# Kernel tuning notes

Hardware: AMD Instinct MI355X
Metric: run time of the kernel (lower is better)

Reference implementation:

```python
import jax, jax.numpy as jnp
import numpy as np

BATCH, NSTEPS, IN_F, OUT_F = 8192, 16, 256, 512


def setup_inputs() -> dict:
    key = jax.random.key(0)
    ks = jax.random.split(key, 20)
    r = jax.random.normal
    return {
        "x": r(ks[0], (BATCH, NSTEPS, IN_F), jnp.float32),
        "C": r(ks[1], (BATCH, OUT_F, 1), jnp.float32),
        "H": r(ks[2], (BATCH, OUT_F, 1), jnp.float32),
        "fg_w_c": r(ks[3], (OUT_F, 1), jnp.float32),
        "fg_w_h": r(ks[4], (OUT_F, OUT_F), jnp.float32),
        "fg_w_x": r(ks[5], (OUT_F, IN_F), jnp.float32),
        "fg_b": r(ks[6], (OUT_F, 1), jnp.float32),
        "ig_w_c": r(ks[7], (OUT_F, 1), jnp.float32),
        "ig_w_h": r(ks[8], (OUT_F, OUT_F), jnp.float32),
        "ig_w_x": r(ks[9], (OUT_F, IN_F), jnp.float32),
        "ig_b": r(ks[10], (OUT_F, 1), jnp.float32),
        "in_w_h": r(ks[11], (OUT_F, OUT_F), jnp.float32),
        "in_w_x": r(ks[12], (OUT_F, IN_F), jnp.float32),
        "in_b": r(ks[13], (OUT_F, 1), jnp.float32),
        "og_w_cn": r(ks[14], (OUT_F, 1), jnp.float32),
        "og_w_h": r(ks[15], (OUT_F, OUT_F), jnp.float32),
        "og_w_x": r(ks[16], (OUT_F, IN_F), jnp.float32),
        "og_b": r(ks[17], (OUT_F, 1), jnp.float32),
        "n": 3,
    }


def reference(x, C, H,
              fg_w_c, fg_w_h, fg_w_x, fg_b,
              ig_w_c, ig_w_h, ig_w_x, ig_b,
              in_w_h, in_w_x, in_b,
              og_w_cn, og_w_h, og_w_x, og_b,
              n):
    # x: [B, T, IN] -> current step [B, IN, 1]
    x_cur = x[:, n, :, None]
    # peephole LSTM gates; matmul broadcasts [O,O] @ [B,O,1] -> [B,O,1]
    fg = jax.nn.sigmoid(fg_w_c * C + jnp.matmul(fg_w_h, H) + jnp.matmul(fg_w_x, x_cur) + fg_b)
    ig = jax.nn.sigmoid(ig_w_c * C + jnp.matmul(ig_w_h, H) + jnp.matmul(ig_w_x, x_cur) + ig_b)
    inn = jnp.tanh(jnp.matmul(in_w_h, H) + jnp.matmul(in_w_x, x_cur) + in_b)
    cm = fg * C + ig * inn
    og = jax.nn.sigmoid(og_w_cn * cm + jnp.matmul(og_w_h, H) + jnp.matmul(og_w_x, x_cur) + og_b)
    h = og * jnp.tanh(cm)
    return (cm, h)
```

## Files before the change

kernel.cpp:

```cpp
#include <hip/hip_runtime.h>


typedef _Float16 half8 __attribute__((ext_vector_type(8)));
typedef _Float16 half4v __attribute__((ext_vector_type(4)));
typedef float floatx4 __attribute__((ext_vector_type(4)));

#define BATCH 8192
#define NSTEPS 16
#define IN_F 256
#define OUT_F 512
#define KDIM 768
#define NDIM 2048

#define BM 128
#define BN 128
#define BK 64

__device__ __forceinline__ void async_copy16(const void* gptr, void* lptr) {
  __builtin_amdgcn_global_load_lds(
      (const __attribute__((address_space(1))) unsigned int*)gptr,
      (__attribute__((address_space(3))) unsigned int*)lptr,
      16, 0, 0);
}

__device__ __forceinline__ float sigmoidf_(float x) {
  return 1.0f / (1.0f + __expf(-x));
}

__device__ __forceinline__ float tanhf_(float x) {
  x = fminf(fmaxf(x, -20.0f), 20.0f);
  float e = __expf(2.0f * x);
  return (e - 1.0f) / (e + 1.0f);
}

__global__ void pack_A(const float* __restrict__ H, const float* __restrict__ x,
                       const int* __restrict__ nptr, _Float16* __restrict__ A) {
  const int n = *nptr;
  const int b = blockIdx.x;
  const int k = threadIdx.x * 4;
  float4 v;
  if (k < OUT_F)
    v = *(const float4*)(H + (size_t)b * OUT_F + k);
  else
    v = *(const float4*)(x + ((size_t)b * NSTEPS + n) * IN_F + (k - OUT_F));
  half4v h = {(_Float16)v.x, (_Float16)v.y, (_Float16)v.z, (_Float16)v.w};
  *(half4v*)(A + (size_t)b * KDIM + k) = h;
}

__global__ void pack_W(const float* __restrict__ fg_w_h, const float* __restrict__ fg_w_x,
                       const float* __restrict__ ig_w_h, const float* __restrict__ ig_w_x,
                       const float* __restrict__ in_w_h, const float* __restrict__ in_w_x,
                       const float* __restrict__ og_w_h, const float* __restrict__ og_w_x,
                       _Float16* __restrict__ W) {
  const int row = blockIdx.x;
  const int g = row >> 9;
  const int j = row & 511;
  const int k = threadIdx.x * 4;
  const float* src;
  if (k < OUT_F) {
    const float* wh = (g == 0) ? fg_w_h : (g == 1) ? ig_w_h : (g == 2) ? in_w_h : og_w_h;
    src = wh + (size_t)j * OUT_F + k;
  } else {
    const float* wx = (g == 0) ? fg_w_x : (g == 1) ? ig_w_x : (g == 2) ? in_w_x : og_w_x;
    src = wx + (size_t)j * IN_F + (k - OUT_F);
  }
  float4 v = *(const float4*)src;
  half4v h = {(_Float16)v.x, (_Float16)v.y, (_Float16)v.z, (_Float16)v.w};
  *(half4v*)(W + (size_t)row * KDIM + k) = h;
}

__global__ __launch_bounds__(256) void gemm_f16(const _Float16* __restrict__ A,
                                                const _Float16* __restrict__ W,
                                                float* __restrict__ Z) {
  __shared__ __align__(16) _Float16 As[BM * BK];
  __shared__ __align__(16) _Float16 Bs[BN * BK];

  const int tid = threadIdx.x;
  const int lane = tid & 63;
  const int wave = tid >> 6;
  const int quad = lane >> 4;
  const int l16 = lane & 15;
  const int m0 = blockIdx.y * BM;
  const int n0 = blockIdx.x * BN;
  const int mw = (wave >> 1) * 64;
  const int nw = (wave & 1) * 64;

  floatx4 acc[4][4] = {};

  for (int kt = 0; kt < KDIM; kt += BK) {
    __syncthreads();
#pragma unroll
    for (int r = 0; r < 4; ++r) {
      const int g = r * 256 + tid;
      const int row = g >> 3;
      const int cl = g & 7;
      const int cg = cl ^ (row & 7);
      async_copy16(A + (size_t)(m0 + row) * KDIM + kt + cg * 8,
                   (_Float16*)As + g * 8);
      async_copy16(W + (size_t)(n0 + row) * KDIM + kt + cg * 8,
                   (_Float16*)Bs + g * 8);
    }
    __syncthreads();

#pragma unroll
    for (int ks = 0; ks < 2; ++ks) {
      half8 af[4], bf[4];
#pragma unroll
      for (int i = 0; i < 4; ++i) {
        const int row = mw + i * 16 + l16;
        const int chunk = ks * 4 + quad;
        const int gran = row * 8 + (chunk ^ (row & 7));
        af[i] = *(const half8*)(As + gran * 8);
      }
#pragma unroll
      for (int j = 0; j < 4; ++j) {
        const int row = nw + j * 16 + l16;
        const int chunk = ks * 4 + quad;
        const int gran = row * 8 + (chunk ^ (row & 7));
        bf[j] = *(const half8*)(Bs + gran * 8);
      }
#pragma unroll
      for (int i = 0; i < 4; ++i)
#pragma unroll
        for (int j = 0; j < 4; ++j)
          acc[i][j] = __builtin_amdgcn_mfma_f32_16x16x32_f16(af[i], bf[j], acc[i][j], 0, 0, 0);
    }
  }

#pragma unroll
  for (int i = 0; i < 4; ++i) {
    const int rbase = m0 + mw + i * 16 + quad * 4;
#pragma unroll
    for (int j = 0; j < 4; ++j) {
      const int col = n0 + nw + j * 16 + l16;
#pragma unroll
      for (int r = 0; r < 4; ++r)
        Z[(size_t)(rbase + r) * NDIM + col] = acc[i][j][r];
    }
  }
}

__global__ void epilogue(const float* __restrict__ Z, const float* __restrict__ C,
                         const float* __restrict__ fg_w_c, const float* __restrict__ fg_b,
                         const float* __restrict__ ig_w_c, const float* __restrict__ ig_b,
                         const float* __restrict__ in_b,
                         const float* __restrict__ og_w_cn, const float* __restrict__ og_b,
                         float* __restrict__ out) {
  const int t = blockIdx.x * 256 + threadIdx.x;
  const int j = (t & 127) << 2;
  const int b = t >> 7;

  const float4 zf = *(const float4*)(Z + (size_t)b * NDIM + j);
  const float4 zi = *(const float4*)(Z + (size_t)b * NDIM + OUT_F + j);
  const float4 zn = *(const float4*)(Z + (size_t)b * NDIM + 2 * OUT_F + j);
  const float4 zo = *(const float4*)(Z + (size_t)b * NDIM + 3 * OUT_F + j);
  const float4 cv = *(const float4*)(C + (size_t)b * OUT_F + j);
  const float4 fwc = *(const float4*)(fg_w_c + j);
  const float4 fb  = *(const float4*)(fg_b + j);
  const float4 iwc = *(const float4*)(ig_w_c + j);
  const float4 ib  = *(const float4*)(ig_b + j);
  const float4 nb  = *(const float4*)(in_b + j);
  const float4 owc = *(const float4*)(og_w_cn + j);
  const float4 ob  = *(const float4*)(og_b + j);

  const float* zfp = (const float*)&zf; const float* zip = (const float*)&zi;
  const float* znp = (const float*)&zn; const float* zop = (const float*)&zo;
  const float* cp  = (const float*)&cv;
  const float* fwcp = (const float*)&fwc; const float* fbp = (const float*)&fb;
  const float* iwcp = (const float*)&iwc; const float* ibp = (const float*)&ib;
  const float* nbp  = (const float*)&nb;
  const float* owcp = (const float*)&owc; const float* obp = (const float*)&ob;

  float4 cm4, h4;
  float* cmp = (float*)&cm4;
  float* hp  = (float*)&h4;
#pragma unroll
  for (int q = 0; q < 4; ++q) {
    const float c = cp[q];
    const float fg = sigmoidf_(fwcp[q] * c + zfp[q] + fbp[q]);
    const float ig = sigmoidf_(iwcp[q] * c + zip[q] + ibp[q]);
    const float inn = tanhf_(znp[q] + nbp[q]);
    const float cm = fg * c + ig * inn;
    const float og = sigmoidf_(owcp[q] * cm + zop[q] + obp[q]);
    cmp[q] = cm;
    hp[q] = og * tanhf_(cm);
  }
  *(float4*)(out + (size_t)b * OUT_F + j) = cm4;
  *(float4*)(out + (size_t)BATCH * OUT_F + (size_t)b * OUT_F + j) = h4;
}

extern "C" void kernel_launch(void* const* d_in, const int* in_sizes, int n_in,
                              void* d_out, int out_size, void* d_ws, size_t ws_size,
                              hipStream_t stream) {
  const float* x       = (const float*)d_in[0];
  const float* C       = (const float*)d_in[1];
  const float* H       = (const float*)d_in[2];
  const float* fg_w_c  = (const float*)d_in[3];
  const float* fg_w_h  = (const float*)d_in[4];
  const float* fg_w_x  = (const float*)d_in[5];
  const float* fg_b    = (const float*)d_in[6];
  const float* ig_w_c  = (const float*)d_in[7];
  const float* ig_w_h  = (const float*)d_in[8];
  const float* ig_w_x  = (const float*)d_in[9];
  const float* ig_b    = (const float*)d_in[10];
  const float* in_w_h  = (const float*)d_in[11];
  const float* in_w_x  = (const float*)d_in[12];
  const float* in_b    = (const float*)d_in[13];
  const float* og_w_cn = (const float*)d_in[14];
  const float* og_w_h  = (const float*)d_in[15];
  const float* og_w_x  = (const float*)d_in[16];
  const float* og_b    = (const float*)d_in[17];
  const int*   nptr    = (const int*)d_in[18];

  char* ws = (char*)d_ws;
  _Float16* Apk = (_Float16*)ws;
  _Float16* Wpk = (_Float16*)(ws + 12582912);
  float*    Z   = (float*)(ws + 15728640);
  (void)ws_size; (void)in_sizes; (void)n_in; (void)out_size;

  pack_A<<<BATCH, 192, 0, stream>>>(H, x, nptr, Apk);
  pack_W<<<NDIM, 192, 0, stream>>>(fg_w_h, fg_w_x, ig_w_h, ig_w_x,
                                   in_w_h, in_w_x, og_w_h, og_w_x, Wpk);
  dim3 grid(NDIM / BN, BATCH / BM);
  gemm_f16<<<grid, 256, 0, stream>>>(Apk, Wpk, Z);
  epilogue<<<(BATCH * OUT_F / 4) / 256, 256, 0, stream>>>(
      Z, C, fg_w_c, fg_b, ig_w_c, ig_b, in_b, og_w_cn, og_b, (float*)d_out);
}
```

Baseline: 283.1 us.

## Fuse LSTM gate epilogue into GEMM by interleaving gate rows in packed weights

```diff
diff --git a/kernel.cpp b/kernel.cpp
--- a/kernel.cpp
+++ b/kernel.cpp
@@ -11,6 +11,7 @@
 #define OUT_F 512
 #define KDIM 768
 #define NDIM 2048
+#define HSIZE ((size_t)BATCH * OUT_F)
 
 #define BM 128
 #define BN 128
@@ -53,25 +54,30 @@
                        const float* __restrict__ og_w_h, const float* __restrict__ og_w_x,
                        _Float16* __restrict__ W) {
   const int row = blockIdx.x;
-  const int g = row >> 9;
-  const int j = row & 511;
+  const int g  = (row >> 4) & 3;
+  const int jj = ((row >> 6) << 4) | (row & 15);
   const int k = threadIdx.x * 4;
   const float* src;
   if (k < OUT_F) {
     const float* wh = (g == 0) ? fg_w_h : (g == 1) ? ig_w_h : (g == 2) ? in_w_h : og_w_h;
-    src = wh + (size_t)j * OUT_F + k;
+    src = wh + (size_t)jj * OUT_F + k;
   } else {
     const float* wx = (g == 0) ? fg_w_x : (g == 1) ? ig_w_x : (g == 2) ? in_w_x : og_w_x;
-    src = wx + (size_t)j * IN_F + (k - OUT_F);
+    src = wx + (size_t)jj * IN_F + (k - OUT_F);
   }
   float4 v = *(const float4*)src;
   half4v h = {(_Float16)v.x, (_Float16)v.y, (_Float16)v.z, (_Float16)v.w};
   *(half4v*)(W + (size_t)row * KDIM + k) = h;
 }
 
-__global__ __launch_bounds__(256) void gemm_f16(const _Float16* __restrict__ A,
-                                                const _Float16* __restrict__ W,
-                                                float* __restrict__ Z) {
+__global__ __launch_bounds__(256) void gemm_lstm(
+    const _Float16* __restrict__ A, const _Float16* __restrict__ W,
+    const float* __restrict__ C,
+    const float* __restrict__ fg_w_c, const float* __restrict__ fg_b,
+    const float* __restrict__ ig_w_c, const float* __restrict__ ig_b,
+    const float* __restrict__ in_b,
+    const float* __restrict__ og_w_cn, const float* __restrict__ og_b,
+    float* __restrict__ out) {
   __shared__ __align__(16) _Float16 As[BM * BK];
   __shared__ __align__(16) _Float16 Bs[BN * BK];
 
@@ -84,6 +90,12 @@
   const int n0 = blockIdx.x * BN;
   const int mw = (wave >> 1) * 64;
   const int nw = (wave & 1) * 64;
+
+  const int jj = (((n0 + nw) >> 6) << 4) | l16;
+  const float fwc = fg_w_c[jj], fb = fg_b[jj];
+  const float iwc = ig_w_c[jj], ib = ig_b[jj];
+  const float nb  = in_b[jj];
+  const float owc = og_w_cn[jj], ob = og_b[jj];
 
   floatx4 acc[4][4] = {};
 
@@ -131,62 +143,18 @@
   for (int i = 0; i < 4; ++i) {
     const int rbase = m0 + mw + i * 16 + quad * 4;
 #pragma unroll
-    for (int j = 0; j < 4; ++j) {
-      const int col = n0 + nw + j * 16 + l16;
-#pragma unroll
-      for (int r = 0; r < 4; ++r)
-        Z[(size_t)(rbase + r) * NDIM + col] = acc[i][j][r];
+    for (int r = 0; r < 4; ++r) {
+      const int b = rbase + r;
+      const float c = C[(size_t)b * OUT_F + jj];
+      const float fg  = sigmoidf_(fwc * c + acc[i][0][r] + fb);
+      const float ig  = sigmoidf_(iwc * c + acc[i][1][r] + ib);
+      const float inn = tanhf_(acc[i][2][r] + nb);
+      const float cm  = fg * c + ig * inn;
+      const float og  = sigmoidf_(owc * cm + acc[i][3][r] + ob);
+      out[(size_t)b * OUT_F + jj] = cm;
+      out[HSIZE + (size_t)b * OUT_F + jj] = og * tanhf_(cm);
     }
   }
-}
-
-__global__ void epilogue(const float* __restrict__ Z, const float* __restrict__ C,
-                         const float* __restrict__ fg_w_c, const float* __restrict__ fg_b,
-                         const float* __restrict__ ig_w_c, const float* __restrict__ ig_b,
-                         const float* __restrict__ in_b,
-                         const float* __restrict__ og_w_cn, const float* __restrict__ og_b,
-                         float* __restrict__ out) {
-  const int t = blockIdx.x * 256 + threadIdx.x;
-  const int j = (t & 127) << 2;
-  const int b = t >> 7;
-
-  const float4 zf = *(const float4*)(Z + (size_t)b * NDIM + j);
-  const float4 zi = *(const float4*)(Z + (size_t)b * NDIM + OUT_F + j);
-  const float4 zn = *(const float4*)(Z + (size_t)b * NDIM + 2 * OUT_F + j);
-  const float4 zo = *(const float4*)(Z + (size_t)b * NDIM + 3 * OUT_F + j);
-  const float4 cv = *(const float4*)(C + (size_t)b * OUT_F + j);
-  const float4 fwc = *(const float4*)(fg_w_c + j);
-  const float4 fb  = *(const float4*)(fg_b + j);
-  const float4 iwc = *(const float4*)(ig_w_c + j);
-  const float4 ib  = *(const float4*)(ig_b + j);
-  const float4 nb  = *(const float4*)(in_b + j);
-  const float4 owc = *(const float4*)(og_w_cn + j);
-  const float4 ob  = *(const float4*)(og_b + j);
-
-  const float* zfp = (const float*)&zf; const float* zip = (const float*)&zi;
-  const float* znp = (const float*)&zn; const float* zop = (const float*)&zo;
-  const float* cp  = (const float*)&cv;
-  const float* fwcp = (const float*)&fwc; const float* fbp = (const float*)&fb;
-  const float* iwcp = (const float*)&iwc; const float* ibp = (const float*)&ib;
-  const float* nbp  = (const float*)&nb;
-  const float* owcp = (const float*)&owc; const float* obp = (const float*)&ob;
-
-  float4 cm4, h4;
-  float* cmp = (float*)&cm4;
-  float* hp  = (float*)&h4;
-#pragma unroll
-  for (int q = 0; q < 4; ++q) {
-    const float c = cp[q];
-    const float fg = sigmoidf_(fwcp[q] * c + zfp[q] + fbp[q]);
-    const float ig = sigmoidf_(iwcp[q] * c + zip[q] + ibp[q]);
-    const float inn = tanhf_(znp[q] + nbp[q]);
-    const float cm = fg * c + ig * inn;
-    const float og = sigmoidf_(owcp[q] * cm + zop[q] + obp[q]);
-    cmp[q] = cm;
-    hp[q] = og * tanhf_(cm);
-  }
-  *(float4*)(out + (size_t)b * OUT_F + j) = cm4;
-  *(float4*)(out + (size_t)BATCH * OUT_F + (size_t)b * OUT_F + j) = h4;
 }
 
 extern "C" void kernel_launch(void* const* d_in, const int* in_sizes, int n_in,
@@ -215,14 +183,13 @@
   char* ws = (char*)d_ws;
   _Float16* Apk = (_Float16*)ws;
   _Float16* Wpk = (_Float16*)(ws + 12582912);
-  float*    Z   = (float*)(ws + 15728640);
   (void)ws_size; (void)in_sizes; (void)n_in; (void)out_size;
 
   pack_A<<<BATCH, 192, 0, stream>>>(H, x, nptr, Apk);
   pack_W<<<NDIM, 192, 0, stream>>>(fg_w_h, fg_w_x, ig_w_h, ig_w_x,
                                    in_w_h, in_w_x, og_w_h, og_w_x, Wpk);
   dim3 grid(NDIM / BN, BATCH / BM);
-  gemm_f16<<<grid, 256, 0, stream>>>(Apk, Wpk, Z);
-  epilogue<<<(BATCH * OUT_F / 4) / 256, 256, 0, stream>>>(
-      Z, C, fg_w_c, fg_b, ig_w_c, ig_b, in_b, og_w_cn, og_b, (float*)d_out);
+  gemm_lstm<<<grid, 256, 0, stream>>>(Apk, Wpk, C,
+                                      fg_w_c, fg_b, ig_w_c, ig_b, in_b,
+                                      og_w_cn, og_b, (float*)d_out);
 }
```

Result: faster. 264.8 us (-6.5%).
